# Kernel optimization log

Hardware: AMD Instinct MI355X
Metric: run time of the kernel (lower is better)

Reference implementation:

```python
import jax, jax.numpy as jnp
import numpy as np

K = 3
PAD = K // 2
EPS = 1e-5


def setup_inputs() -> dict:
    key = jax.random.key(0)
    k1, k2, k3 = jax.random.split(key, 3)
    B, C, H, W = 16, 256, 56, 56
    x = jax.random.normal(k1, (B, C, H, W), jnp.float32)
    offset = jax.random.normal(k2, (B, 2 * K * K, H, W), jnp.float32)  # matches torch.randn offsets
    weight = jax.random.normal(k3, (C, C, K, K), jnp.float32) * (1.0 / np.sqrt(C * K * K))
    gamma = jnp.ones((C,), jnp.float32)
    beta = jnp.zeros((C,), jnp.float32)
    return {"x": x, "offset": offset, "weight": weight, "gamma": gamma, "beta": beta}


def _bilinear_sample(x, py, px):
    # x: [B,C,H,W]; py,px: [B,H,W] fractional sample coords; zero padding outside.
    B, C, H, W = x.shape
    y0 = jnp.floor(py)
    x0 = jnp.floor(px)
    wy1 = py - y0  # weight for y0+1
    wx1 = px - x0
    wy0 = 1.0 - wy1
    wx0 = 1.0 - wx1
    x_flat = x.reshape(B, C, H * W)

    def corner(yc, xc, w):
        valid = ((yc >= 0) & (yc <= H - 1) & (xc >= 0) & (xc <= W - 1)).astype(x.dtype)
        yi = jnp.clip(yc, 0, H - 1).astype(jnp.int32)
        xi = jnp.clip(xc, 0, W - 1).astype(jnp.int32)
        idx = (yi * W + xi).reshape(B, 1, H * W)
        v = jnp.take_along_axis(x_flat, jnp.broadcast_to(idx, (B, C, H * W)), axis=2)
        return v.reshape(B, C, H, W) * (w * valid)[:, None, :, :]

    return (corner(y0, x0, wy0 * wx0) + corner(y0, x0 + 1, wy0 * wx1)
            + corner(y0 + 1, x0, wy1 * wx0) + corner(y0 + 1, x0 + 1, wy1 * wx1))


def _deform_conv(x, offset, weight):
    B, C, H, W = x.shape
    base_y = jnp.arange(H, dtype=x.dtype)[None, :, None]  # [1,H,1]
    base_x = jnp.arange(W, dtype=x.dtype)[None, None, :]  # [1,1,W]
    out = jnp.zeros((B, weight.shape[0], H, W), x.dtype)
    for k in range(K * K):  # fixed small loop over kernel taps
        kh, kw = k // K, k % K
        py = base_y + (kh - PAD) + offset[:, 2 * k]
        px = base_x + (kw - PAD) + offset[:, 2 * k + 1]
        samp = _bilinear_sample(x, py, px)  # [B,C,H,W]
        out = out + jnp.einsum('bchw,oc->bohw', samp, weight[:, :, kh, kw])
    return out


def reference(x, offset, weight, gamma, beta):
    y = _deform_conv(x, offset, weight)
    mean = y.mean(axis=(0, 2, 3))
    var = y.var(axis=(0, 2, 3))  # biased var, training-mode BN
    yhat = (y - mean[:, None, None]) * jax.lax.rsqrt(var[:, None, None] + EPS)
    return jax.nn.relu(yhat * gamma[:, None, None] + beta[:, None, None])
```

## Files before the change

kernel.cpp:

```cpp
#include <hip/hip_runtime.h>
#include <stdint.h>

#define HW    3136
#define CH    256
#define NBAT  16
#define RDIM  2304
#define NPOS  50176
#define EPSV  1e-5f
#define NBLK  784
#define NCOL  1568

typedef __bf16 bf16x8 __attribute__((ext_vector_type(8)));
typedef float  f32x4  __attribute__((ext_vector_type(4)));
typedef unsigned int u32x4 __attribute__((ext_vector_type(4)));

__device__ __forceinline__ unsigned short f2bf(float f) {
    union { float f; unsigned int u; } z; z.f = f;
    unsigned int u = z.u;
    u += 0x7FFFu + ((u >> 16) & 1u);
    return (unsigned short)(u >> 16);
}

__device__ __forceinline__ unsigned int cvtpk(float lo, float hi) {
    unsigned int r;
    asm("v_cvt_pk_bf16_f32 %0, %1, %2" : "=v"(r) : "v"(lo), "v"(hi));
    return r;
}

__device__ __forceinline__ void gload_lds16(const void* g, void* l) {
    __builtin_amdgcn_global_load_lds(
        (const __attribute__((address_space(1))) unsigned int*)g,
        (__attribute__((address_space(3))) unsigned int*)l,
        16, 0, 0);
}

__global__ __launch_bounds__(256) void k_transpose(const float* __restrict__ x,
                                                   unsigned short* __restrict__ xt) {
    __shared__ float tile[64][65];
    int hw0 = blockIdx.x * 64;
    int c0  = blockIdx.y * 64;
    int b   = blockIdx.z;
    int tx = threadIdx.x & 63;
    int ty = threadIdx.x >> 6;
    const float* xp = x + ((size_t)(b * CH + c0)) * HW + hw0;
#pragma unroll
    for (int i = 0; i < 16; i++) {
        int c_l = ty + i * 4;
        tile[c_l][tx] = xp[(size_t)c_l * HW + tx];
    }
    __syncthreads();
    unsigned short* op = xt + ((size_t)(b * HW + hw0)) * CH + c0;
#pragma unroll
    for (int i = 0; i < 16; i++) {
        int hw_l = ty + i * 4;
        op[(size_t)hw_l * CH + tx] = f2bf(tile[tx][hw_l]);
    }
}

__global__ __launch_bounds__(256) void k_w2(const float* __restrict__ w,
                                            unsigned short* __restrict__ w2) {
    int idx = blockIdx.x * 256 + threadIdx.x;
    int c = idx & 255;
    int k = (idx >> 8) % 9;
    int o = idx / RDIM;
    w2[idx] = f2bf(w[o * RDIM + c * 9 + k]);
}

#define BK 64
__global__ __launch_bounds__(512) void k_fgemm(const unsigned short* __restrict__ xt,
                                               const float* __restrict__ off,
                                               const unsigned short* __restrict__ W2,
                                               float* __restrict__ y,
                                               float* __restrict__ psum_s,
                                               float* __restrict__ psum_q) {
    __shared__ __align__(16) unsigned short lA[256 * BK];
    __shared__ __align__(16) unsigned short lB[64 * BK];
    __shared__ float2 smeta[4][64];
    int t    = threadIdx.x;
    int wid  = t >> 6;
    int lane = t & 63;
    int n0   = blockIdx.x * 64;
    int b    = blockIdx.y;
    const unsigned short* xb = xt + (size_t)b * HW * CH;

    int m_off = (wid >> 1) * 64;
    int n_off = (wid & 1) * 32;
    int fr = lane & 15;
    int fq = lane >> 4;

    int bp  = t >> 3;
    int bcg = t & 7;
    unsigned short* lbdst = &lB[bp * BK + ((bcg ^ (bp & 7)) * 8)];

    f32x4 acc[4][2];
#pragma unroll
    for (int m = 0; m < 4; m++)
#pragma unroll
        for (int n = 0; n < 2; n++)
            acc[m][n] = (f32x4){0.f, 0.f, 0.f, 0.f};

    for (int tap = 0; tap < 9; tap++) {
        if (t < 64) {
            int hw = n0 + t;
            int h = hw / 56, w = hw - h * 56;
            float offY = off[((size_t)(b * 18 + 2 * tap)) * HW + hw];
            float offX = off[((size_t)(b * 18 + 2 * tap + 1)) * HW + hw];
            float py = (float)(h + tap / 3 - 1) + offY;
            float px = (float)(w + tap % 3 - 1) + offX;
            float y0f = floorf(py), x0f = floorf(px);
            float fy = py - y0f, fx = px - x0f;
            float wy[2] = {1.f - fy, fy};
            float wx[2] = {1.f - fx, fx};
#pragma unroll
            for (int j = 0; j < 4; j++) {
                int dy = j >> 1, dx = j & 1;
                float ycf = y0f + (float)dy, xcf = x0f + (float)dx;
                bool v = (ycf >= 0.f) && (ycf <= 55.f) && (xcf >= 0.f) && (xcf <= 55.f);
                int yi = min(max((int)ycf, 0), 55);
                int xi = min(max((int)xcf, 0), 55);
                float wgt = v ? wy[dy] * wx[dx] : 0.f;
                smeta[j][t] = make_float2(__int_as_float(yi * 56 + xi), wgt);
            }
        }
        __syncthreads();
        int   cidx[4];
        float cwgt[4];
#pragma unroll
        for (int j = 0; j < 4; j++) {
            float2 m2 = smeta[j][bp];
            cidx[j] = __float_as_int(m2.x);
            cwgt[j] = m2.y;
        }

#pragma unroll
        for (int kk4 = 0; kk4 < 4; kk4++) {
            int r0 = tap * 256 + kk4 * 64;
#pragma unroll
            for (int i = 0; i < 4; i++) {
                int q = t + 512 * i;
                int row = q >> 3;
                int part = (q & 7) ^ (row & 7);
                gload_lds16(W2 + (size_t)row * RDIM + r0 + part * 8,
                            &lA[(size_t)(wid * 64 + 512 * i) * 8]);
            }
            {
                int c0 = kk4 * 64 + bcg * 8;
                float al[4] = {0.f, 0.f, 0.f, 0.f};
                float ah[4] = {0.f, 0.f, 0.f, 0.f};
#pragma unroll
                for (int j = 0; j < 4; j++) {
                    u32x4 cv = *(const u32x4*)(xb + (size_t)cidx[j] * CH + c0);
                    float wj = cwgt[j];
#pragma unroll
                    for (int i = 0; i < 4; i++) {
                        float lo = __uint_as_float(cv[i] << 16);
                        float hi = __uint_as_float(cv[i] & 0xffff0000u);
                        al[i] = fmaf(wj, lo, al[i]);
                        ah[i] = fmaf(wj, hi, ah[i]);
                    }
                }
                u32x4 ov;
#pragma unroll
                for (int i = 0; i < 4; i++) ov[i] = cvtpk(al[i], ah[i]);
                *(u32x4*)lbdst = ov;
            }
            __syncthreads();
#pragma unroll
            for (int kk = 0; kk < 2; kk++) {
                bf16x8 afr[4], bfr[2];
#pragma unroll
                for (int m = 0; m < 4; m++) {
                    int row = m_off + m * 16 + fr;
                    int slot = (kk * 4 + fq) ^ (row & 7);
                    afr[m] = *(const bf16x8*)&lA[row * BK + slot * 8];
                }
#pragma unroll
                for (int n = 0; n < 2; n++) {
                    int row = n_off + n * 16 + fr;
                    int slot = (kk * 4 + fq) ^ (row & 7);
                    bfr[n] = *(const bf16x8*)&lB[row * BK + slot * 8];
                }
#pragma unroll
                for (int m = 0; m < 4; m++)
#pragma unroll
                    for (int n = 0; n < 2; n++)
                        acc[m][n] = __builtin_amdgcn_mfma_f32_16x16x32_bf16(afr[m], bfr[n], acc[m][n], 0, 0, 0);
            }
            __syncthreads();
        }
    }

    float* yb = y + (size_t)b * CH * HW;
#pragma unroll
    for (int m = 0; m < 4; m++) {
        int o = m_off + m * 16 + fq * 4;
#pragma unroll
        for (int n = 0; n < 2; n++) {
            int p = n0 + n_off + n * 16 + fr;
#pragma unroll
            for (int j = 0; j < 4; j++)
                yb[(size_t)(o + j) * HW + p] = acc[m][n][j];
        }
    }

    int blk2 = (b * 49 + blockIdx.x) * 2 + (wid & 1);
#pragma unroll
    for (int m = 0; m < 4; m++)
#pragma unroll
        for (int j = 0; j < 4; j++) {
            float s = acc[m][0][j] + acc[m][1][j];
            float q = acc[m][0][j] * acc[m][0][j] + acc[m][1][j] * acc[m][1][j];
#pragma unroll
            for (int msk = 1; msk < 16; msk <<= 1) {
                s += __shfl_xor(s, msk);
                q += __shfl_xor(q, msk);
            }
            if (fr == 0) {
                int o = m_off + m * 16 + fq * 4 + j;
                psum_s[(size_t)o * NCOL + blk2] = s;
                psum_q[(size_t)o * NCOL + blk2] = q;
            }
        }
}

__global__ __launch_bounds__(256) void k_stats2(const float* __restrict__ psum_s,
                                                const float* __restrict__ psum_q,
                                                const float* __restrict__ gamma,
                                                const float* __restrict__ beta,
                                                float* __restrict__ scaleArr,
                                                float* __restrict__ shiftArr) {
    int o = blockIdx.x;
    int t = threadIdx.x;
    float s = 0.f, q = 0.f;
    for (int i = t; i < NCOL; i += 256) {
        s += psum_s[(size_t)o * NCOL + i];
        q += psum_q[(size_t)o * NCOL + i];
    }
    __shared__ float r1[256], r2[256];
    r1[t] = s; r2[t] = q;
    __syncthreads();
    for (int st = 128; st > 0; st >>= 1) {
        if (t < st) { r1[t] += r1[t + st]; r2[t] += r2[t + st]; }
        __syncthreads();
    }
    if (t == 0) {
        float inv = 1.f / (float)NPOS;
        float mean = r1[0] * inv;
        float var  = r2[0] * inv - mean * mean;
        float sc = gamma[o] * rsqrtf(var + EPSV);
        scaleArr[o] = sc;
        shiftArr[o] = beta[o] - mean * sc;
    }
}

__global__ __launch_bounds__(256) void k_norm(float* __restrict__ y,
                                              const float* __restrict__ scaleArr,
                                              const float* __restrict__ shiftArr) {
    const int total4 = NBAT * CH * (HW / 4);
    for (int i = blockIdx.x * 256 + threadIdx.x; i < total4; i += gridDim.x * 256) {
        int o = (i / (HW / 4)) & 255;
        float sc = scaleArr[o], sh = shiftArr[o];
        float4 v = ((const float4*)y)[i];
        float4 r;
        r.x = fmaxf(v.x * sc + sh, 0.f);
        r.y = fmaxf(v.y * sc + sh, 0.f);
        r.z = fmaxf(v.z * sc + sh, 0.f);
        r.w = fmaxf(v.w * sc + sh, 0.f);
        ((float4*)y)[i] = r;
    }
}

extern "C" void kernel_launch(void* const* d_in, const int* in_sizes, int n_in,
                              void* d_out, int out_size, void* d_ws, size_t ws_size,
                              hipStream_t stream) {
    const float* x     = (const float*)d_in[0];
    const float* off   = (const float*)d_in[1];
    const float* wgt   = (const float*)d_in[2];
    const float* gamma = (const float*)d_in[3];
    const float* beta  = (const float*)d_in[4];
    float* out = (float*)d_out;
    char* ws = (char*)d_ws;

    unsigned short* W2 = (unsigned short*)(ws + 0);
    unsigned short* xt = (unsigned short*)(ws + 1179648);
    float* psum_s      = (float*)(ws + 26869760);
    float* psum_q      = (float*)(ws + 28475392);
    float* scaleArr    = (float*)(ws + 30081024);
    float* shiftArr    = (float*)(ws + 30082048);

    k_transpose<<<dim3(49, 4, 16), 256, 0, stream>>>(x, xt);
    k_w2<<<2304, 256, 0, stream>>>(wgt, W2);
    k_fgemm<<<dim3(49, 16), 512, 0, stream>>>(xt, off, W2, out, psum_s, psum_q);
    k_stats2<<<256, 256, 0, stream>>>(psum_s, psum_q, gamma, beta, scaleArr, shiftArr);
    k_norm<<<2048, 256, 0, stream>>>(out, scaleArr, shiftArr);
}
```

Measured before the change: 190.5 us.

## Remap fgemm blocks per XCD, compute sample metadata per thread, hoist gathers

```diff
diff --git a/kernel.cpp b/kernel.cpp
--- a/kernel.cpp
+++ b/kernel.cpp
@@ -7,7 +7,6 @@
 #define RDIM  2304
 #define NPOS  50176
 #define EPSV  1e-5f
-#define NBLK  784
 #define NCOL  1568
 
 typedef __bf16 bf16x8 __attribute__((ext_vector_type(8)));
@@ -67,20 +66,24 @@
 }
 
 #define BK 64
-__global__ __launch_bounds__(512) void k_fgemm(const unsigned short* __restrict__ xt,
-                                               const float* __restrict__ off,
-                                               const unsigned short* __restrict__ W2,
-                                               float* __restrict__ y,
-                                               float* __restrict__ psum_s,
-                                               float* __restrict__ psum_q) {
+__global__ __launch_bounds__(512, 8) void k_fgemm(const unsigned short* __restrict__ xt,
+                                                  const float* __restrict__ off,
+                                                  const unsigned short* __restrict__ W2,
+                                                  float* __restrict__ y,
+                                                  float* __restrict__ psum_s,
+                                                  float* __restrict__ psum_q) {
     __shared__ __align__(16) unsigned short lA[256 * BK];
     __shared__ __align__(16) unsigned short lB[64 * BK];
-    __shared__ float2 smeta[4][64];
     int t    = threadIdx.x;
     int wid  = t >> 6;
     int lane = t & 63;
-    int n0   = blockIdx.x * 64;
-    int b    = blockIdx.y;
+
+    int bid  = blockIdx.x;
+    int xcd  = bid & 7;
+    int j    = bid >> 3;
+    int b    = 2 * xcd + (j >= 49 ? 1 : 0);
+    int spat = (j >= 49) ? j - 49 : j;
+    int n0   = spat * 64;
     const unsigned short* xb = xt + (size_t)b * HW * CH;
 
     int m_off = (wid >> 1) * 64;
@@ -90,6 +93,8 @@
 
     int bp  = t >> 3;
     int bcg = t & 7;
+    int hw = n0 + bp;
+    int h = hw / 56, w = hw - h * 56;
     unsigned short* lbdst = &lB[bp * BK + ((bcg ^ (bp & 7)) * 8)];
 
     f32x4 acc[4][2];
@@ -100,9 +105,9 @@
             acc[m][n] = (f32x4){0.f, 0.f, 0.f, 0.f};
 
     for (int tap = 0; tap < 9; tap++) {
-        if (t < 64) {
-            int hw = n0 + t;
-            int h = hw / 56, w = hw - h * 56;
+        int   cidx[4];
+        float cwgt[4];
+        {
             float offY = off[((size_t)(b * 18 + 2 * tap)) * HW + hw];
             float offX = off[((size_t)(b * 18 + 2 * tap + 1)) * HW + hw];
             float py = (float)(h + tap / 3 - 1) + offY;
@@ -112,29 +117,25 @@
             float wy[2] = {1.f - fy, fy};
             float wx[2] = {1.f - fx, fx};
 #pragma unroll
-            for (int j = 0; j < 4; j++) {
-                int dy = j >> 1, dx = j & 1;
+            for (int jj = 0; jj < 4; jj++) {
+                int dy = jj >> 1, dx = jj & 1;
                 float ycf = y0f + (float)dy, xcf = x0f + (float)dx;
                 bool v = (ycf >= 0.f) && (ycf <= 55.f) && (xcf >= 0.f) && (xcf <= 55.f);
                 int yi = min(max((int)ycf, 0), 55);
                 int xi = min(max((int)xcf, 0), 55);
-                float wgt = v ? wy[dy] * wx[dx] : 0.f;
-                smeta[j][t] = make_float2(__int_as_float(yi * 56 + xi), wgt);
-            }
-        }
-        __syncthreads();
-        int   cidx[4];
-        float cwgt[4];
-#pragma unroll
-        for (int j = 0; j < 4; j++) {
-            float2 m2 = smeta[j][bp];
-            cidx[j] = __float_as_int(m2.x);
-            cwgt[j] = m2.y;
+                cidx[jj] = yi * 56 + xi;
+                cwgt[jj] = v ? wy[dy] * wx[dx] : 0.f;
+            }
         }
 
 #pragma unroll
         for (int kk4 = 0; kk4 < 4; kk4++) {
             int r0 = tap * 256 + kk4 * 64;
+            int c0 = kk4 * 64 + bcg * 8;
+            u32x4 cv0 = *(const u32x4*)(xb + (size_t)cidx[0] * CH + c0);
+            u32x4 cv1 = *(const u32x4*)(xb + (size_t)cidx[1] * CH + c0);
+            u32x4 cv2 = *(const u32x4*)(xb + (size_t)cidx[2] * CH + c0);
+            u32x4 cv3 = *(const u32x4*)(xb + (size_t)cidx[3] * CH + c0);
 #pragma unroll
             for (int i = 0; i < 4; i++) {
                 int q = t + 512 * i;
@@ -144,20 +145,19 @@
                             &lA[(size_t)(wid * 64 + 512 * i) * 8]);
             }
             {
-                int c0 = kk4 * 64 + bcg * 8;
                 float al[4] = {0.f, 0.f, 0.f, 0.f};
                 float ah[4] = {0.f, 0.f, 0.f, 0.f};
 #pragma unroll
-                for (int j = 0; j < 4; j++) {
-                    u32x4 cv = *(const u32x4*)(xb + (size_t)cidx[j] * CH + c0);
-                    float wj = cwgt[j];
-#pragma unroll
-                    for (int i = 0; i < 4; i++) {
-                        float lo = __uint_as_float(cv[i] << 16);
-                        float hi = __uint_as_float(cv[i] & 0xffff0000u);
-                        al[i] = fmaf(wj, lo, al[i]);
-                        ah[i] = fmaf(wj, hi, ah[i]);
-                    }
+                for (int i = 0; i < 4; i++) {
+                    float w0 = cwgt[0], w1 = cwgt[1], w2v = cwgt[2], w3 = cwgt[3];
+                    al[i] = fmaf(w0, __uint_as_float(cv0[i] << 16),
+                            fmaf(w1, __uint_as_float(cv1[i] << 16),
+                            fmaf(w2v, __uint_as_float(cv2[i] << 16),
+                                 w3 * __uint_as_float(cv3[i] << 16))));
+                    ah[i] = fmaf(w0, __uint_as_float(cv0[i] & 0xffff0000u),
+                            fmaf(w1, __uint_as_float(cv1[i] & 0xffff0000u),
+                            fmaf(w2v, __uint_as_float(cv2[i] & 0xffff0000u),
+                                 w3 * __uint_as_float(cv3[i] & 0xffff0000u))));
                 }
                 u32x4 ov;
 #pragma unroll
@@ -165,6 +165,7 @@
                 *(u32x4*)lbdst = ov;
             }
             __syncthreads();
+            __builtin_amdgcn_s_setprio(1);
 #pragma unroll
             for (int kk = 0; kk < 2; kk++) {
                 bf16x8 afr[4], bfr[2];
@@ -186,6 +187,7 @@
                     for (int n = 0; n < 2; n++)
                         acc[m][n] = __builtin_amdgcn_mfma_f32_16x16x32_bf16(afr[m], bfr[n], acc[m][n], 0, 0, 0);
             }
+            __builtin_amdgcn_s_setprio(0);
             __syncthreads();
         }
     }
@@ -198,25 +200,25 @@
         for (int n = 0; n < 2; n++) {
             int p = n0 + n_off + n * 16 + fr;
 #pragma unroll
-            for (int j = 0; j < 4; j++)
-                yb[(size_t)(o + j) * HW + p] = acc[m][n][j];
-        }
-    }
-
-    int blk2 = (b * 49 + blockIdx.x) * 2 + (wid & 1);
+            for (int jj = 0; jj < 4; jj++)
+                yb[(size_t)(o + jj) * HW + p] = acc[m][n][jj];
+        }
+    }
+
+    int blk2 = (b * 49 + spat) * 2 + (wid & 1);
 #pragma unroll
     for (int m = 0; m < 4; m++)
 #pragma unroll
-        for (int j = 0; j < 4; j++) {
-            float s = acc[m][0][j] + acc[m][1][j];
-            float q = acc[m][0][j] * acc[m][0][j] + acc[m][1][j] * acc[m][1][j];
+        for (int jj = 0; jj < 4; jj++) {
+            float s = acc[m][0][jj] + acc[m][1][jj];
+            float q = acc[m][0][jj] * acc[m][0][jj] + acc[m][1][jj] * acc[m][1][jj];
 #pragma unroll
             for (int msk = 1; msk < 16; msk <<= 1) {
                 s += __shfl_xor(s, msk);
                 q += __shfl_xor(q, msk);
             }
             if (fr == 0) {
-                int o = m_off + m * 16 + fq * 4 + j;
+                int o = m_off + m * 16 + fq * 4 + jj;
                 psum_s[(size_t)o * NCOL + blk2] = s;
                 psum_q[(size_t)o * NCOL + blk2] = q;
             }
@@ -290,7 +292,7 @@
 
     k_transpose<<<dim3(49, 4, 16), 256, 0, stream>>>(x, xt);
     k_w2<<<2304, 256, 0, stream>>>(wgt, W2);
-    k_fgemm<<<dim3(49, 16), 512, 0, stream>>>(xt, off, W2, out, psum_s, psum_q);
+    k_fgemm<<<784, 512, 0, stream>>>(xt, off, W2, out, psum_s, psum_q);
     k_stats2<<<256, 256, 0, stream>>>(psum_s, psum_q, gamma, beta, scaleArr, shiftArr);
     k_norm<<<2048, 256, 0, stream>>>(out, scaleArr, shiftArr);
 }
```

After: 385.5 us. 102% more time.
